# Kernel optimization log

Measured on AMD Instinct MI355X. Metric: run time of the kernel, lower is better.

## Reference

```python
import jax, jax.numpy as jnp
import numpy as np

D_MODEL = 1024
N_HEAD = 16
HEAD_DIM = D_MODEL // N_HEAD


def setup_inputs() -> dict:
    key = jax.random.key(0)
    ks = jax.random.split(key, 11)
    B, S = 2, 2048
    scale = 1.0 / np.sqrt(D_MODEL)
    inp = {
        'q': jax.random.normal(ks[0], (B, S, D_MODEL), dtype=jnp.float32),
        'k': jax.random.normal(ks[1], (B, S, D_MODEL), dtype=jnp.float32),
        'v': jax.random.normal(ks[2], (B, S, D_MODEL), dtype=jnp.float32),
        'Wq': jax.random.normal(ks[3], (D_MODEL, D_MODEL), dtype=jnp.float32) * scale,
        'bq': jnp.zeros((D_MODEL,), dtype=jnp.float32),
        'Wk': jax.random.normal(ks[4], (D_MODEL, D_MODEL), dtype=jnp.float32) * scale,
        'bk': jnp.zeros((D_MODEL,), dtype=jnp.float32),
        'Wv': jax.random.normal(ks[5], (D_MODEL, D_MODEL), dtype=jnp.float32) * scale,
        'bv': jnp.zeros((D_MODEL,), dtype=jnp.float32),
        'Wo': jax.random.normal(ks[6], (D_MODEL, D_MODEL), dtype=jnp.float32) * scale,
        'bo': jnp.zeros((D_MODEL,), dtype=jnp.float32),
    }
    return inp


def _split_heads(x):
    # [B, S, D] -> [B, H, S, Dh]
    B, S, _ = x.shape
    return x.reshape(B, S, N_HEAD, HEAD_DIM).transpose(0, 2, 1, 3)


def reference(q, k, v, Wq, bq, Wk, bk, Wv, bv, Wo, bo):
    B, S, _ = q.shape
    qh = _split_heads(q @ Wq + bq)  # [B,H,S,Dh]
    kh = _split_heads(k @ Wk + bk)
    vh = _split_heads(v @ Wv + bv)
    inv_sqrt_d = jnp.asarray(1.0 / np.sqrt(HEAD_DIM), dtype=q.dtype)
    scores = jnp.einsum('bhqd,bhkd->bhqk', qh, kh) * inv_sqrt_d  # [B,H,S,S]
    attn = jax.nn.softmax(scores, axis=-1)
    out = jnp.einsum('bhqk,bhkd->bhqd', attn, vh)  # [B,H,S,Dh]
    out = out.transpose(0, 2, 1, 3).reshape(B, S, D_MODEL)
    return out @ Wo + bo
```

## Files before the change

### kernel.cpp

```cpp
#include <hip/hip_runtime.h>
#include <cstdint>
#include <cstddef>

#define D_MODEL 1024
#define NHEAD 16
#define HDIM 64
#define BATCH 2
#define SEQ 2048
#define MROWS (BATCH*SEQ)

typedef _Float16 f16;
typedef _Float16 f16x2 __attribute__((ext_vector_type(2)));
typedef _Float16 f16x4 __attribute__((ext_vector_type(4)));
typedef _Float16 f16x8 __attribute__((ext_vector_type(8)));
typedef float f32x4 __attribute__((ext_vector_type(4)));
typedef __fp16 fp16x2_raw __attribute__((ext_vector_type(2)));

__device__ __forceinline__ f16x2 cvt_pk(float a, float b) {
  fp16x2_raw t = __builtin_amdgcn_cvt_pkrtz(a, b);
  return __builtin_bit_cast(f16x2, t);
}

__device__ __forceinline__ float fast_exp2(float x) {
  return __builtin_amdgcn_exp2f(x);
}

#define QSCALE 0.18033688011112042f
#define CSHIFT 6.0f

__device__ __forceinline__ void gload_lds16(const void* gsrc, void* ldst) {
  __builtin_amdgcn_global_load_lds(
      (__attribute__((address_space(1))) void*)gsrc,
      (__attribute__((address_space(3))) void*)ldst,
      16, 0, 0);
}

__global__ __launch_bounds__(256) void prep_kernel(
    const float* __restrict__ q, const float* __restrict__ k,
    const float* __restrict__ v, f16* __restrict__ Xf,
    const float* __restrict__ W0, const float* __restrict__ W1,
    const float* __restrict__ W2, const float* __restrict__ W3,
    f16* __restrict__ T0, f16* __restrict__ T1,
    f16* __restrict__ T2, f16* __restrict__ T3) {
  __shared__ float tile[32][33];
  const int id = blockIdx.x;
  if (id < 6144) {
    const int z = id >> 11;
    const int bx = id & 2047;
    const float* in = (z == 0) ? q : (z == 1) ? k : v;
    f16* out = Xf + (size_t)z * MROWS * D_MODEL;
    int i = (bx * 256 + threadIdx.x) * 8;
    const float4* p = (const float4*)(in + i);
    float4 a = p[0], b = p[1];
    f16x8 o = { (f16)a.x,(f16)a.y,(f16)a.z,(f16)a.w,
                (f16)b.x,(f16)b.y,(f16)b.z,(f16)b.w };
    *(f16x8*)(out + i) = o;
  } else {
    const int jj = id - 6144;
    const int z = jj >> 10;
    const int rem = jj & 1023;
    const int n0 = (rem & 31) * 32, k0 = (rem >> 5) * 32;
    const float* W = (z == 0) ? W0 : (z == 1) ? W1 : (z == 2) ? W2 : W3;
    f16* Wt = (z == 0) ? T0 : (z == 1) ? T1 : (z == 2) ? T2 : T3;
    const int tx = threadIdx.x & 31, ty = threadIdx.x >> 5;
    #pragma unroll
    for (int j = 0; j < 32; j += 8)
      tile[ty + j][tx] = W[(size_t)(k0 + ty + j) * D_MODEL + n0 + tx];
    __syncthreads();
    #pragma unroll
    for (int j = 0; j < 32; j += 8)
      Wt[(size_t)(n0 + ty + j) * D_MODEL + k0 + tx] = (f16)tile[tx][ty + j];
  }
}

__global__ __launch_bounds__(256, 3) void gemm_qkv(
    const f16* __restrict__ Xf,
    const f16* __restrict__ Wtq, const f16* __restrict__ Wtk, const f16* __restrict__ Wtv,
    const float* __restrict__ bq, const float* __restrict__ bk, const float* __restrict__ bv,
    f16* __restrict__ Qh, f16* __restrict__ Kf, f16* __restrict__ Vf) {
  __shared__ __align__(16) f16 As[128 * 64];
  __shared__ __align__(16) f16 Bs[128 * 64];
  const int id = blockIdx.x;
  const int xcd = id & 7;
  const int s5 = id >> 3;
  const int bn_i = s5 & 7;
  const int t5 = xcd * 12 + (s5 >> 3);
  const int z = t5 >> 5;
  const int bm_i = t5 & 31;
  const int bm = bm_i * 128, bn = bn_i * 128;
  const f16* A  = Xf + (size_t)z * MROWS * D_MODEL + (size_t)bm * 1024;
  const f16* Bt = ((z == 0) ? Wtq : (z == 1) ? Wtk : Wtv) + (size_t)bn * 1024;
  const float* bias = (z == 0) ? bq : (z == 1) ? bk : bv;
  const int tid = threadIdx.x, wave = tid >> 6, lane = tid & 63;
  const int lr = lane & 15, lq = lane >> 4, sw = lr & 7;
  const int wm = (wave >> 1) * 64, wn = (wave & 1) * 64;
  const int srow = lane >> 3;
  const int scs  = (lane & 7) ^ srow;
  const f16* Ag = A  + (size_t)(wave * 32 + srow) * 1024 + scs * 8;
  const f16* Bg = Bt + (size_t)(wave * 32 + srow) * 1024 + scs * 8;

  f32x4 acc[4][4];
  #pragma unroll
  for (int i = 0; i < 4; i++)
    #pragma unroll
    for (int j = 0; j < 4; j++) acc[i][j] = (f32x4){0.f, 0.f, 0.f, 0.f};

  for (int k0 = 0; k0 < 1024; k0 += 64) {
    __syncthreads();
    #pragma unroll
    for (int g = 0; g < 4; g++) {
      gload_lds16(Ag + (size_t)g * 8 * 1024 + k0, As + wave * 2048 + g * 512);
      gload_lds16(Bg + (size_t)g * 8 * 1024 + k0, Bs + wave * 2048 + g * 512);
    }
    __syncthreads();
    #pragma unroll
    for (int t = 0; t < 2; t++) {
      f16x8 af[4], bf[4];
      #pragma unroll
      for (int m = 0; m < 4; m++)
        af[m] = *(const f16x8*)(As + (size_t)(wm + m * 16 + lr) * 64 + (((t * 4 + lq) ^ sw) * 8));
      #pragma unroll
      for (int j = 0; j < 4; j++)
        bf[j] = *(const f16x8*)(Bs + (size_t)(wn + j * 16 + lr) * 64 + (((t * 4 + lq) ^ sw) * 8));
      #pragma unroll
      for (int m = 0; m < 4; m++)
        #pragma unroll
        for (int j = 0; j < 4; j++)
          acc[m][j] = __builtin_amdgcn_mfma_f32_16x16x32_f16(af[m], bf[j], acc[m][j], 0, 0, 0);
    }
  }

  if (z == 2) {
    const int b = bm >> 11;
    const int hh = (bn + wn) >> 6;
    const size_t bh = (size_t)b * NHEAD + hh;
    const int tile = ((bm & 2047) >> 6) + (wave >> 1);
    #pragma unroll
    for (int j = 0; j < 4; j++) {
      const int col = bn + wn + j * 16 + lr;
      const float bj = bias[col];
      #pragma unroll
      for (int mb = 0; mb < 2; mb++) {
        f16x8 u = { (f16)(acc[mb][j][0] + bj),     (f16)(acc[mb][j][1] + bj),
                    (f16)(acc[mb][j][2] + bj),     (f16)(acc[mb][j][3] + bj),
                    (f16)(acc[mb + 2][j][0] + bj), (f16)(acc[mb + 2][j][1] + bj),
                    (f16)(acc[mb + 2][j][2] + bj), (f16)(acc[mb + 2][j][3] + bj) };
        *(f16x8*)(Vf + ((bh * 32 + tile) * 8 + j * 2 + mb) * 512 + lane * 8) = u;
      }
    }
  } else {
    #pragma unroll
    for (int j = 0; j < 4; j++) {
      const int col = bn + wn + j * 16 + lr;
      const float bj = bias[col];
      const int hh = col >> 6, d = col & 63;
      #pragma unroll
      for (int m = 0; m < 4; m++) {
        #pragma unroll
        for (int r = 0; r < 4; r++) {
          const int row = bm + wm + m * 16 + lq * 4 + r;
          float val = acc[m][j][r] + bj;
          if (z == 0) val *= QSCALE;
          const int b = row >> 11, s = row & 2047;
          const size_t bh = (size_t)b * NHEAD + hh;
          const int tile = s >> 6;
          if (z == 0) {
            Qh[(bh * SEQ + s) * HDIM + d] = (f16)val;
          } else {
            const int kk = s & 63;
            const int f = ((kk >> 4) << 1) | (d >> 5);
            const int ln = ((d >> 3) & 3) * 16 + (kk & 15);
            Kf[((bh * 32 + tile) * 8 + f) * 512 + ln * 8 + (d & 7)] = (f16)val;
          }
        }
      }
    }
  }
}

__global__ __launch_bounds__(256, 4) void gemm_o(
    const f16* __restrict__ AO, const f16* __restrict__ Wto,
    const float* __restrict__ bo, float* __restrict__ out) {
  __shared__ __align__(16) f16 As[64 * 64];
  __shared__ __align__(16) f16 Bs[128 * 64];
  const int id = blockIdx.x;
  const int xcd = id & 7;
  const int s5 = id >> 3;
  const int bn_i = s5 & 7;
  const int bm_i = xcd * 8 + (s5 >> 3);
  const int bm = bm_i * 64, bn = bn_i * 128;
  const int tid = threadIdx.x, wave = tid >> 6, lane = tid & 63;
  const int lr = lane & 15, lq = lane >> 4, sw = lr & 7;
  const int wm = (wave >> 1) * 32, wn = (wave & 1) * 64;
  const int srow = lane >> 3;
  const int scs  = (lane & 7) ^ srow;
  const f16* Ag = AO  + (size_t)(bm + wave * 16 + srow) * 1024 + scs * 8;
  const f16* Bg = Wto + (size_t)(bn + wave * 32 + srow) * 1024 + scs * 8;

  f32x4 acc[2][4];
  #pragma unroll
  for (int i = 0; i < 2; i++)
    #pragma unroll
    for (int j = 0; j < 4; j++) acc[i][j] = (f32x4){0.f, 0.f, 0.f, 0.f};

  for (int k0 = 0; k0 < 1024; k0 += 64) {
    __syncthreads();
    #pragma unroll
    for (int g = 0; g < 2; g++)
      gload_lds16(Ag + (size_t)g * 8 * 1024 + k0, As + wave * 1024 + g * 512);
    #pragma unroll
    for (int g = 0; g < 4; g++)
      gload_lds16(Bg + (size_t)g * 8 * 1024 + k0, Bs + wave * 2048 + g * 512);
    __syncthreads();
    #pragma unroll
    for (int t = 0; t < 2; t++) {
      f16x8 af[2], bf[4];
      #pragma unroll
      for (int m = 0; m < 2; m++)
        af[m] = *(const f16x8*)(As + (size_t)(wm + m * 16 + lr) * 64 + (((t * 4 + lq) ^ sw) * 8));
      #pragma unroll
      for (int j = 0; j < 4; j++)
        bf[j] = *(const f16x8*)(Bs + (size_t)(wn + j * 16 + lr) * 64 + (((t * 4 + lq) ^ sw) * 8));
      #pragma unroll
      for (int m = 0; m < 2; m++)
        #pragma unroll
        for (int j = 0; j < 4; j++)
          acc[m][j] = __builtin_amdgcn_mfma_f32_16x16x32_f16(af[m], bf[j], acc[m][j], 0, 0, 0);
    }
  }
  #pragma unroll
  for (int j = 0; j < 4; j++) {
    const int col = bn + wn + j * 16 + lr;
    const float bj = bo[col];
    #pragma unroll
    for (int m = 0; m < 2; m++)
      #pragma unroll
      for (int r = 0; r < 4; r++) {
        const int row = bm + wm + m * 16 + lq * 4 + r;
        out[(size_t)row * D_MODEL + col] = acc[m][j][r] + bj;
      }
  }
}

__global__ __launch_bounds__(256, 2) void flash_kernel(
    const f16* __restrict__ Qh, const f16* __restrict__ Kf,
    const f16* __restrict__ Vf, f16* __restrict__ AO) {
  __shared__ __align__(16) f16 Ks[2][8 * 512];
  const int id = blockIdx.x;
  const int xcd = id & 7;
  const int s6 = id >> 3;
  const int q_i = s6 & 15;
  const int hl = xcd * 4 + (s6 >> 4);
  const int h = hl & 15, b = hl >> 4;
  const int tid = threadIdx.x, wave = tid >> 6, lane = tid & 63;
  const int lr = lane & 15, lq = lane >> 4;
  const size_t bh = (size_t)b * NHEAD + h;
  const f16* Qb = Qh + bh * SEQ * HDIM;
  const f16* Kb = Kf + bh * 32 * 4096 + lane * 8;
  const f16* Vb = Vf + bh * 32 * 4096 + lane * 8;
  const int q0 = q_i * 128 + wave * 32;

  f16x8 aq[2][2];
  #pragma unroll
  for (int m = 0; m < 2; m++)
    #pragma unroll
    for (int t = 0; t < 2; t++)
      aq[m][t] = *(const f16x8*)(Qb + (size_t)(q0 + m * 16 + lr) * HDIM + t * 32 + lq * 8);

  f32x4 oacc[2][4], ls[2];
  #pragma unroll
  for (int m = 0; m < 2; m++) {
    ls[m] = (f32x4){0.f, 0.f, 0.f, 0.f};
    #pragma unroll
    for (int j = 0; j < 4; j++) oacc[m][j] = (f32x4){0.f, 0.f, 0.f, 0.f};
  }
  const f32x4 mC = {-CSHIFT, -CSHIFT, -CSHIFT, -CSHIFT};
  const f16x8 ones = {(f16)1, (f16)1, (f16)1, (f16)1, (f16)1, (f16)1, (f16)1, (f16)1};

  f16x8 vvA[8], vvB[8];

  #define FITER(it, CUR, VVC, VVN, PF, PVW)                                    \
    do {                                                                       \
      if (PF) {                                                                \
        gload_lds16(Kb + ((size_t)((it) + 1) * 8 + 2 * wave) * 512,            \
                    &Ks[(CUR) ^ 1][(2 * wave) * 512]);                         \
        gload_lds16(Kb + ((size_t)((it) + 1) * 8 + 2 * wave + 1) * 512,        \
                    &Ks[(CUR) ^ 1][(2 * wave + 1) * 512]);                     \
        __builtin_amdgcn_sched_barrier(0);                                     \
        _Pragma("unroll")                                                      \
        for (int f = 0; f < 8; f++)                                            \
          VVN[f] = *(const f16x8*)(Vb + ((size_t)((it) + 1) * 8 + f) * 512);   \
      }                                                                        \
      __builtin_amdgcn_sched_barrier(0);                                       \
      f32x4 sc[4][2];                                                          \
      _Pragma("unroll")                                                        \
      for (int t = 0; t < 2; t++) {                                            \
        f16x8 bk[4];                                                           \
        _Pragma("unroll")                                                      \
        for (int j = 0; j < 4; j++)                                            \
          bk[j] = *(const f16x8*)(&Ks[CUR][(j * 2 + t) * 512 + lane * 8]);     \
        _Pragma("unroll")                                                      \
        for (int j = 0; j < 4; j++)                                            \
          _Pragma("unroll")                                                    \
          for (int m = 0; m < 2; m++)                                          \
            sc[j][m] = __builtin_amdgcn_mfma_f32_16x16x32_f16(                 \
                bk[j], aq[m][t], (t == 0) ? mC : sc[j][m], 0, 0, 0);           \
      }                                                                        \
      f16x8 ap[2][2];                                                          \
      _Pragma("unroll")                                                        \
      for (int m = 0; m < 2; m++)                                              \
        _Pragma("unroll")                                                      \
        for (int t = 0; t < 2; t++) {                                          \
          union { f16x8 v; f16x2 h2[4]; } u;                                   \
          const f32x4 lo = sc[t][m], hi = sc[t + 2][m];                        \
          u.h2[0] = cvt_pk(fast_exp2(lo[0]), fast_exp2(lo[1]));                \
          u.h2[1] = cvt_pk(fast_exp2(lo[2]), fast_exp2(lo[3]));                \
          u.h2[2] = cvt_pk(fast_exp2(hi[0]), fast_exp2(hi[1]));                \
          u.h2[3] = cvt_pk(fast_exp2(hi[2]), fast_exp2(hi[3]));                \
          ap[m][t] = u.v;                                                      \
        }                                                                      \
      asm volatile("s_waitcnt vmcnt(" #PVW ")" ::: "memory");                  \
      __builtin_amdgcn_sched_barrier(0);                                       \
      _Pragma("unroll")                                                        \
      for (int t = 0; t < 2; t++) {                                            \
        _Pragma("unroll")                                                      \
        for (int j = 0; j < 4; j++)                                            \
          _Pragma("unroll")                                                    \
          for (int m = 0; m < 2; m++)                                          \
            oacc[m][j] = __builtin_amdgcn_mfma_f32_16x16x32_f16(               \
                ap[m][t], VVC[j * 2 + t], oacc[m][j], 0, 0, 0);                \
        _Pragma("unroll")                                                      \
        for (int m = 0; m < 2; m++)                                            \
          ls[m] = __builtin_amdgcn_mfma_f32_16x16x32_f16(                      \
              ap[m][t], ones, ls[m], 0, 0, 0);                                 \
      }                                                                        \
      if (PF) {                                                                \
        asm volatile("s_waitcnt vmcnt(8)" ::: "memory");                       \
        __builtin_amdgcn_s_barrier();                                          \
        __builtin_amdgcn_sched_barrier(0);                                     \
      }                                                                        \
    } while (0)

  gload_lds16(Kb + (size_t)(2 * wave) * 512, &Ks[0][(2 * wave) * 512]);
  gload_lds16(Kb + (size_t)(2 * wave + 1) * 512, &Ks[0][(2 * wave + 1) * 512]);
  #pragma unroll
  for (int f = 0; f < 8; f++)
    vvA[f] = *(const f16x8*)(Vb + (size_t)f * 512);
  __syncthreads();

  for (int it2 = 0; it2 < 15; it2++) {
    FITER(it2 * 2,     0, vvA, vvB, 1, 10);
    FITER(it2 * 2 + 1, 1, vvB, vvA, 1, 10);
  }
  FITER(30, 0, vvA, vvB, 1, 10);
  FITER(31, 1, vvB, vvA, 0, 0);
  #undef FITER

  #pragma unroll
  for (int m = 0; m < 2; m++)
    #pragma unroll
    for (int r = 0; r < 4; r++) {
      const float inv = 1.0f / ls[m][r];
      const int row = q0 + m * 16 + lq * 4 + r;
      #pragma unroll
      for (int j = 0; j < 4; j++) {
        const int col = h * HDIM + j * 16 + lr;
        AO[((size_t)b * SEQ + row) * D_MODEL + col] = (f16)(oacc[m][j][r] * inv);
      }
    }
}

extern "C" void kernel_launch(void* const* d_in, const int* in_sizes, int n_in,
                              void* d_out, int out_size, void* d_ws, size_t ws_size,
                              hipStream_t stream) {
  const float* q  = (const float*)d_in[0];
  const float* k  = (const float*)d_in[1];
  const float* v  = (const float*)d_in[2];
  const float* Wq = (const float*)d_in[3];
  const float* bq = (const float*)d_in[4];
  const float* Wk = (const float*)d_in[5];
  const float* bk = (const float*)d_in[6];
  const float* Wv = (const float*)d_in[7];
  const float* bv = (const float*)d_in[8];
  const float* Wo = (const float*)d_in[9];
  const float* bo = (const float*)d_in[10];
  float* out = (float*)d_out;

  char* ws = (char*)d_ws;
  f16* Wt_q = (f16*)(ws + ((size_t)0  << 20));
  f16* Wt_k = (f16*)(ws + ((size_t)2  << 20));
  f16* Wt_v = (f16*)(ws + ((size_t)4  << 20));
  f16* Wt_o = (f16*)(ws + ((size_t)6  << 20));
  f16* Xf   = (f16*)(ws + ((size_t)8  << 20));
  f16* Qh_  = (f16*)(ws + ((size_t)32 << 20));
  f16* Kf_  = (f16*)(ws + ((size_t)40 << 20));
  f16* Vf_  = (f16*)(ws + ((size_t)48 << 20));
  f16* AO   = Xf;

  prep_kernel<<<10240, 256, 0, stream>>>(
      q, k, v, Xf, Wq, Wk, Wv, Wo, Wt_q, Wt_k, Wt_v, Wt_o);

  gemm_qkv<<<768, 256, 0, stream>>>(
      Xf, Wt_q, Wt_k, Wt_v, bq, bk, bv, Qh_, Kf_, Vf_);

  flash_kernel<<<512, 256, 0, stream>>>(Qh_, Kf_, Vf_, AO);

  gemm_o<<<512, 256, 0, stream>>>(AO, Wt_o, bo, out);
}
```

Baseline: 201.4 us.

## Stage Q/K epilogue through LDS for coalesced fragment-layout stores

```diff
diff --git a/kernel.cpp b/kernel.cpp
--- a/kernel.cpp
+++ b/kernel.cpp
@@ -78,8 +78,9 @@
     const f16* __restrict__ Wtq, const f16* __restrict__ Wtk, const f16* __restrict__ Wtv,
     const float* __restrict__ bq, const float* __restrict__ bk, const float* __restrict__ bv,
     f16* __restrict__ Qh, f16* __restrict__ Kf, f16* __restrict__ Vf) {
-  __shared__ __align__(16) f16 As[128 * 64];
-  __shared__ __align__(16) f16 Bs[128 * 64];
+  __shared__ __align__(16) f16 SMEM[2 * 128 * 64];
+  f16* As = SMEM;
+  f16* Bs = SMEM + 128 * 64;
   const int id = blockIdx.x;
   const int xcd = id & 7;
   const int s5 = id >> 3;
@@ -130,11 +131,13 @@
     }
   }
 
+  const int brow = bm + wm;
+  const int b = brow >> 11;
+  const int tile = (brow & 2047) >> 6;
+  const int hh = (bn + wn) >> 6;
+  const size_t bh = (size_t)b * NHEAD + hh;
+
   if (z == 2) {
-    const int b = bm >> 11;
-    const int hh = (bn + wn) >> 6;
-    const size_t bh = (size_t)b * NHEAD + hh;
-    const int tile = ((bm & 2047) >> 6) + (wave >> 1);
     #pragma unroll
     for (int j = 0; j < 4; j++) {
       const int col = bn + wn + j * 16 + lr;
@@ -149,31 +152,32 @@
       }
     }
   } else {
-    #pragma unroll
-    for (int j = 0; j < 4; j++) {
-      const int col = bn + wn + j * 16 + lr;
-      const float bj = bias[col];
-      const int hh = col >> 6, d = col & 63;
-      #pragma unroll
-      for (int m = 0; m < 4; m++) {
+    __syncthreads();
+    f16* Lw = SMEM + wave * 4096;
+    #pragma unroll
+    for (int m = 0; m < 4; m++)
+      #pragma unroll
+      for (int j = 0; j < 4; j++) {
+        const int col = bn + wn + j * 16 + lr;
+        const float bj = bias[col];
+        const int dcol = j * 16 + lr;
         #pragma unroll
         for (int r = 0; r < 4; r++) {
-          const int row = bm + wm + m * 16 + lq * 4 + r;
           float val = acc[m][j][r] + bj;
           if (z == 0) val *= QSCALE;
-          const int b = row >> 11, s = row & 2047;
-          const size_t bh = (size_t)b * NHEAD + hh;
-          const int tile = s >> 6;
-          if (z == 0) {
-            Qh[(bh * SEQ + s) * HDIM + d] = (f16)val;
-          } else {
-            const int kk = s & 63;
-            const int f = ((kk >> 4) << 1) | (d >> 5);
-            const int ln = ((d >> 3) & 3) * 16 + (kk & 15);
-            Kf[((bh * 32 + tile) * 8 + f) * 512 + ln * 8 + (d & 7)] = (f16)val;
-          }
+          const int row = m * 16 + lq * 4 + r;
+          Lw[row * 64 + (((dcol >> 3) ^ (row & 7)) * 8) + (dcol & 7)] = (f16)val;
         }
       }
+    f16* dst = ((z == 0) ? Qh : Kf) + ((bh * 32 + tile) * 8) * 512;
+    #pragma unroll
+    for (int f = 0; f < 8; f++) {
+      const int row = (z == 0)
+          ? ((f >> 2) & 1) * 32 + ((f >> 1) & 1) * 16 + lr
+          : (f >> 1) * 16 + lr;
+      const int colc = (f & 1) * 4 + lq;
+      f16x8 u = *(const f16x8*)(Lw + row * 64 + ((colc ^ (row & 7)) * 8));
+      *(f16x8*)(dst + f * 512 + lane * 8) = u;
     }
   }
 }
@@ -255,17 +259,21 @@
   const int tid = threadIdx.x, wave = tid >> 6, lane = tid & 63;
   const int lr = lane & 15, lq = lane >> 4;
   const size_t bh = (size_t)b * NHEAD + h;
-  const f16* Qb = Qh + bh * SEQ * HDIM;
   const f16* Kb = Kf + bh * 32 * 4096 + lane * 8;
   const f16* Vb = Vf + bh * 32 * 4096 + lane * 8;
   const int q0 = q_i * 128 + wave * 32;
 
   f16x8 aq[2][2];
-  #pragma unroll
-  for (int m = 0; m < 2; m++)
-    #pragma unroll
-    for (int t = 0; t < 2; t++)
-      aq[m][t] = *(const f16x8*)(Qb + (size_t)(q0 + m * 16 + lr) * HDIM + t * 32 + lq * 8);
+  {
+    const int qtile = q0 >> 6;
+    const int qb = (q0 >> 5) & 1;
+    const f16* Qf = Qh + bh * 32 * 4096 + ((size_t)qtile * 8) * 512 + lane * 8;
+    #pragma unroll
+    for (int m = 0; m < 2; m++)
+      #pragma unroll
+      for (int t = 0; t < 2; t++)
+        aq[m][t] = *(const f16x8*)(Qf + (qb * 4 + m * 2 + t) * 512);
+  }
 
   f32x4 oacc[2][4], ls[2];
   #pragma unroll
```

Result: no change. 201.1 us (median of 3 runs) (-0.1%).
